# Kernel optimization log

Hardware: AMD Instinct MI355X
Metric: run time of the kernel (lower is better)

## Reference

```python
import jax, jax.numpy as jnp
import numpy as np
from jax import lax

N_NODES = 5000; N_EDGES = 160000; N_FEAT = 128; HIDDEN = 256
N_TPL = 10; N_TPL_NODES = 10; N_CLASSES = 8
ALPHA = 0.5          # FGW structure/feature trade-off
CG_ITERS = 5         # conditional-gradient (Frank-Wolfe) outer iterations
SINK_ITERS = 30      # log-domain Sinkhorn iterations (EMD surrogate)
SINK_REG = 0.02      # entropic reg relative to cost scale


def setup_inputs() -> dict:
    key = jax.random.key(0)
    ks = jax.random.split(key, 8)
    x = jax.random.normal(ks[0], (N_NODES, N_FEAT), jnp.float32)
    edge_index = jax.random.randint(ks[1], (2, N_EDGES), 0, N_NODES)
    W1 = jax.random.normal(ks[2], (N_FEAT, HIDDEN), jnp.float32) / np.sqrt(N_FEAT)
    b1 = jnp.zeros((HIDDEN,), jnp.float32)
    W2 = jax.random.normal(ks[3], (HIDDEN, N_FEAT), jnp.float32) / np.sqrt(HIDDEN)
    b2 = jnp.zeros((N_FEAT,), jnp.float32)
    templates = jax.random.uniform(ks[4], (N_TPL, N_TPL_NODES, N_TPL_NODES), jnp.float32)
    templates_features = jax.random.uniform(ks[5], (N_TPL, N_TPL_NODES, N_FEAT), jnp.float32)
    Wlin = jax.random.normal(ks[6], (N_TPL, N_CLASSES), jnp.float32) / np.sqrt(N_TPL)
    blin = jnp.zeros((N_CLASSES,), jnp.float32)
    return dict(x=x, edge_index=edge_index, W1=W1, b1=b1, W2=W2, b2=b2,
                templates=templates, templates_features=templates_features,
                Wlin=Wlin, blin=blin)


def gcn_conv(x, src, dst, W, b):
    # PyG GCNConv: x @ W, then D^-1/2 (A + I) D^-1/2 aggregation, then + b
    n = x.shape[0]
    loop = jnp.arange(n)
    s = jnp.concatenate([src, loop]); d = jnp.concatenate([dst, loop])
    deg = jax.ops.segment_sum(jnp.ones(s.shape[0], x.dtype), d, num_segments=n)
    dinv = lax.rsqrt(jnp.maximum(deg, 1.0))
    h = x @ W
    msg = h[s] * (dinv[s] * dinv[d])[:, None]
    return jax.ops.segment_sum(msg, d, num_segments=n) + b


def sinkhorn_log(G, logp, logq):
    # entropic OT in log domain as a jit-friendly surrogate for exact EMD
    scale = lax.stop_gradient(jnp.max(jnp.abs(G)) + 1e-9)
    mlogK = -G / (SINK_REG * scale)          # [n, m]
    f0 = jnp.zeros(G.shape[0], G.dtype); g0 = jnp.zeros(G.shape[1], G.dtype)
    def body(carry, _):
        f, g = carry
        g = logq - jax.nn.logsumexp(mlogK + f[:, None], axis=0)
        f = logp - jax.nn.logsumexp(mlogK + g[None, :], axis=1)
        return (f, g), None
    (f, g), _ = lax.scan(body, (f0, g0), None, length=SINK_ITERS)
    return jnp.exp(f[:, None] + mlogK + g[None, :])


def fgw2(C1, x, C2, F2):
    # Fused Gromov-Wasserstein distance (square loss), uniform weights,
    # conditional-gradient with fixed step 2/(t+2) and Sinkhorn LP surrogate.
    n, m = C1.shape[0], C2.shape[0]
    p = jnp.full((n,), 1.0 / n, x.dtype); q = jnp.full((m,), 1.0 / m, x.dtype)
    logp = jnp.log(p); logq = jnp.log(q)
    # squared-euclidean feature cost  [n, m]
    M = jnp.sum(x * x, 1)[:, None] + jnp.sum(F2 * F2, 1)[None, :] - 2.0 * x @ F2.T
    # square-loss GW decomposition: f1=a^2, f2=b^2, h1=a, h2=2b
    constC = ((C1 * C1) @ p)[:, None] + ((C2 * C2) @ q)[None, :]
    def tens(T):
        return constC - C1 @ T @ (2.0 * C2).T
    T = p[:, None] * q[None, :]
    for t in range(CG_ITERS):
        grad = (1.0 - ALPHA) * M + 2.0 * ALPHA * tens(T)
        Tnew = sinkhorn_log(grad, logp, logq)
        T = T + (2.0 / (t + 2.0)) * (Tnew - T)
    return (1.0 - ALPHA) * jnp.sum(M * T) + ALPHA * jnp.sum(tens(T) * T)


def reference(x, edge_index, W1, b1, W2, b2, templates, templates_features, Wlin, blin):
    src, dst = edge_index[0], edge_index[1]
    h = jax.nn.relu(gcn_conv(x, src, dst, W1, b1))
    h = gcn_conv(h, src, dst, W2, b2)           # [N, F]
    n = x.shape[0]
    C = jnp.zeros((n, n), x.dtype).at[src, dst].set(1.0)   # dense adjacency
    dists = jax.vmap(lambda Ct, Ft: fgw2(C, h, Ct, Ft))(templates, templates_features)  # [K]
    return dists @ Wlin + blin                  # [num_classes]
```

## Files before the change

kernel.cpp:

```cpp
#include <hip/hip_runtime.h>
#include <cstdint>

#define NND 5000
#define NE 160000
#define NF 128
#define NH 256
#define NT 10
#define MT 10
#define NC 8
#define NMAT (NND*MT)
#define CG_ITERS 5
#define SINK_IT 30

#if __has_builtin(__builtin_amdgcn_update_dpp)
#define DPP_ADD(x, ctrl, rmask) \
    ((x) + __int_as_float(__builtin_amdgcn_update_dpp(0, __float_as_int(x), (ctrl), (rmask), 0xf, true)))
__device__ __forceinline__ float wave_sum63(float x) {
    x = DPP_ADD(x, 0x111, 0xf);
    x = DPP_ADD(x, 0x112, 0xf);
    x = DPP_ADD(x, 0x114, 0xf);
    x = DPP_ADD(x, 0x118, 0xf);
    x = DPP_ADD(x, 0x142, 0xa);
    x = DPP_ADD(x, 0x143, 0xc);
    return x;
}
#else
__device__ __forceinline__ float wave_sum63(float x) {
#pragma unroll
    for (int off = 32; off; off >>= 1) x += __shfl_xor(x, off);
    return x;
}
#endif

__device__ __forceinline__ float frcp(float x) {
#if __has_builtin(__builtin_amdgcn_rcpf)
    return __builtin_amdgcn_rcpf(x);
#else
    return 1.f / x;
#endif
}


__global__ void k_edge1(const int* __restrict__ src, const int* __restrict__ dst,
                        int* __restrict__ cntD, unsigned* __restrict__ bitmap,
                        int* __restrict__ cntS, unsigned char* __restrict__ keep) {
    for (int e = blockIdx.x*blockDim.x + threadIdx.x; e < NE; e += gridDim.x*blockDim.x) {
        int s = src[e], d = dst[e];
        atomicAdd(&cntD[d], 1);
        int key = s * NND + d;
        unsigned bit = 1u << (key & 31);
        unsigned old = atomicOr(&bitmap[key >> 5], bit);
        if (!(old & bit)) { keep[e] = 1; atomicAdd(&cntS[s], 1); }
        else keep[e] = 0;
    }
}

__global__ void k_exscan2(const int* __restrict__ cntD, int* __restrict__ rpD,
                          float* __restrict__ dinv,
                          const int* __restrict__ cntS, int* __restrict__ rpS,
                          float* __restrict__ c1row,
                          const float* __restrict__ tpl, float* __restrict__ c2row) {
    const int T = 1024;
    int tid = threadIdx.x;
    if (blockIdx.x == 2) {
        if (tid < NT * MT) {
            int t = tid / MT, j = tid % MT;
            float s = 0.f;
            for (int k = 0; k < MT; k++) { float v = tpl[t * 100 + j * 10 + k]; s += v * v; }
            c2row[tid] = s * (1.f / MT);
        }
        return;
    }
    const int* cnt = blockIdx.x ? cntS : cntD;
    int* rp = blockIdx.x ? rpS : rpD;
    int C = (NND + T - 1) / T;
    int begin = tid * C, end = begin + C; if (end > NND) end = NND; if (begin > NND) begin = NND;
    int s = 0;
    for (int i = begin; i < end; i++) s += cnt[i];
    __shared__ int part[1024];
    part[tid] = s; __syncthreads();
    for (int off = 1; off < T; off <<= 1) {
        int v = (tid >= off) ? part[tid - off] : 0;
        __syncthreads();
        part[tid] += v;
        __syncthreads();
    }
    int run = part[tid] - s;
    for (int i = begin; i < end; i++) { rp[i] = run; run += cnt[i]; }
    if (tid == T - 1) rp[NND] = part[T - 1];
    if (blockIdx.x == 0)
        for (int i = begin; i < end; i++) dinv[i] = rsqrtf((float)(cnt[i] + 1));
    else
        for (int i = begin; i < end; i++) c1row[i] = (float)cnt[i] * (1.f / NND);
}

__global__ void k_scatter2(const int* __restrict__ src, const int* __restrict__ dst,
                           const unsigned char* __restrict__ keep,
                           const int* __restrict__ rpD, int* __restrict__ cur1,
                           int* __restrict__ csrS, float* __restrict__ csrC,
                           const float* __restrict__ dinv,
                           const int* __restrict__ rpS, int* __restrict__ cur2,
                           int* __restrict__ csrD) {
    for (int e = blockIdx.x*blockDim.x + threadIdx.x; e < NE; e += gridDim.x*blockDim.x) {
        int s = src[e], d = dst[e];
        int pos = rpD[d] + atomicAdd(&cur1[d], 1);
        csrS[pos] = s;
        csrC[pos] = dinv[s] * dinv[d];
        if (keep[e]) {
            int p2 = rpS[s] + atomicAdd(&cur2[s], 1);
            csrD[p2] = d;
        }
    }
}


__global__ __launch_bounds__(256) void k_gemm(const float* __restrict__ A,
                                              const float* __restrict__ B,
                                              float* __restrict__ C, int M, int N, int K,
                                              const float* __restrict__ bias, int relu) {
    const int BM = 64, BN = 64, BK = 16;
    __shared__ float As[BK][BM + 1];
    __shared__ float Bs[BK][BN];
    int tid = threadIdx.x;
    int row0 = blockIdx.y * BM, col0 = blockIdx.x * BN;
    int tx = tid % 16, ty = tid / 16;
    float acc[4][4] = {};
    for (int k0 = 0; k0 < K; k0 += BK) {
#pragma unroll
        for (int l = 0; l < 4; l++) {
            int idx = tid + l * 256;
            int r = idx / BK, kk = idx % BK;
            int gr = row0 + r;
            As[kk][r] = (gr < M) ? A[(size_t)gr * K + k0 + kk] : 0.f;
        }
#pragma unroll
        for (int l = 0; l < 4; l++) {
            int idx = tid + l * 256;
            int kk = idx / BN, c = idx % BN;
            Bs[kk][c] = B[(size_t)(k0 + kk) * N + col0 + c];
        }
        __syncthreads();
#pragma unroll
        for (int kk = 0; kk < BK; kk++) {
            float a[4], b[4];
#pragma unroll
            for (int i = 0; i < 4; i++) a[i] = As[kk][ty * 4 + i];
#pragma unroll
            for (int j = 0; j < 4; j++) b[j] = Bs[kk][tx * 4 + j];
#pragma unroll
            for (int i = 0; i < 4; i++)
#pragma unroll
                for (int j = 0; j < 4; j++) acc[i][j] += a[i] * b[j];
        }
        __syncthreads();
    }
#pragma unroll
    for (int i = 0; i < 4; i++) {
        int gr = row0 + ty * 4 + i;
        if (gr < M) {
#pragma unroll
            for (int j = 0; j < 4; j++) {
                int gc = col0 + tx * 4 + j;
                float o = acc[i][j];
                if (bias) o += bias[gc];
                if (relu) o = fmaxf(o, 0.f);
                C[(size_t)gr * N + gc] = o;
            }
        }
    }
}

__global__ __launch_bounds__(128) void k_aggregate(const float* __restrict__ hin,
                            const float* __restrict__ bias,
                            float* __restrict__ hout, const int* __restrict__ rp,
                            const int* __restrict__ csrS, const float* __restrict__ csrC,
                            const float* __restrict__ dinv) {
    int v = blockIdx.x;
    int f = threadIdx.x;
    float dv = dinv[v];
    float acc = hin[(size_t)v * NF + f] * dv * dv;
    int e0 = rp[v], e1 = rp[v + 1];
    for (int e = e0; e < e1; e++)
        acc += hin[(size_t)csrS[e] * NF + f] * csrC[e];
    if (bias) acc += bias[f];
    hout[(size_t)v * NF + f] = acc;
}


__global__ __launch_bounds__(128) void k_M(const float* __restrict__ h,
                    const float* __restrict__ tplF,
                    float* __restrict__ Mout) {
    int i = blockIdx.x;
    int tid = threadIdx.x;
    int lane = tid & 63, w = tid >> 6;
    __shared__ float hrow[NF];
    __shared__ float part[2];
    float hv = h[(size_t)i * NF + tid];
    hrow[tid] = hv;
    float ps = wave_sum63(hv * hv);
    if (lane == 63) part[w] = ps;
    __syncthreads();
    float sx = part[0] + part[1];
    int c = tid;
    if (c < NT * MT) {
        const float* Fc = tplF + (size_t)c * NF;
        float dot = 0.f, nrm = 0.f;
        for (int f = 0; f < NF; f++) {
            float fv = Fc[f];
            dot = fmaf(hrow[f], fv, dot);
            nrm = fmaf(fv, fv, nrm);
        }
        int t = c / MT, j = c % MT;
        Mout[(size_t)t * NMAT + (size_t)i * MT + j] = sx + nrm - 2.f * dot;
    }
}

__global__ void k_Tinit(float* __restrict__ T) {
    for (int idx = blockIdx.x*blockDim.x + threadIdx.x; idx < NT * NMAT; idx += gridDim.x*blockDim.x)
        T[idx] = 1.f / (float)NMAT;
}


__global__ __launch_bounds__(256) void k_grad(const float* __restrict__ T, const float* __restrict__ Mm,
                                              const float* __restrict__ c1row, const float* __restrict__ c2row,
                                              const float* __restrict__ tpl,
                                              const int* __restrict__ rpS, const int* __restrict__ csrD,
                                              float* __restrict__ G, unsigned* __restrict__ scaleBits) {
    int t = blockIdx.y;
    int tid = threadIdx.x;
    __shared__ float tC2[100];
    if (tid < 100) tC2[tid] = 2.f * tpl[t * 100 + tid];
    __syncthreads();
    int i = blockIdx.x * 256 + tid;
    float amax = 0.f;
    if (i < NND) {
        const float* Tt = T + (size_t)t * NMAT;
        const float* Mt = Mm + (size_t)t * NMAT;
        float* Gt = G + (size_t)t * NMAT;
        float L[MT];
#pragma unroll
        for (int j = 0; j < MT; j++) L[j] = 0.f;
        int e0 = rpS[i], e1 = rpS[i + 1];
        for (int e = e0; e < e1; e++) {
            int k = csrD[e];
            const float* Tk = Tt + (size_t)k * MT;
#pragma unroll
            for (int j = 0; j < MT; j++) L[j] += Tk[j];
        }
        float c1 = c1row[i];
#pragma unroll
        for (int j = 0; j < MT; j++) {
            float s = 0.f;
#pragma unroll
            for (int k = 0; k < MT; k++) s += L[k] * tC2[j * 10 + k];
            float g = 0.5f * Mt[(size_t)i * MT + j] + (c1 + c2row[t * 10 + j] - s);
            Gt[(size_t)i * MT + j] = g;
            amax = fmaxf(amax, fabsf(g));
        }
    }
    __shared__ float red[256];
    red[tid] = amax; __syncthreads();
    for (int off = 128; off > 0; off >>= 1) {
        if (tid < off) red[tid] = fmaxf(red[tid], red[tid + off]);
        __syncthreads();
    }
    if (tid == 0) atomicMax(&scaleBits[t], __float_as_uint(red[0]));
}

__global__ __launch_bounds__(512)
__attribute__((amdgpu_waves_per_eu(1, 2)))
void k_sinkhorn(const float* __restrict__ G,
                const unsigned* __restrict__ scaleBits,
                float* __restrict__ T, float step) {
    int t = blockIdx.x;
    int tid = threadIdx.x;
    int lane = tid & 63, w = tid >> 6;
    float sc = __uint_as_float(scaleBits[t]) + 1e-9f;
    float inv = -1.f / (0.02f * sc);
    const float* Gt = G + (size_t)t * NMAT;
    float* Tt = T + (size_t)t * NMAT;

    __shared__ float wred[8][10];
    __shared__ float vbc[12];

    float Kf[10][10];
    float u[10];
#pragma unroll
    for (int r = 0; r < 10; r++) {
        int i = tid + r * 512;
        if (i < NND) {
            u[r] = 1.f;
            const float2* Gr = (const float2*)(Gt + (size_t)i * 10);
#pragma unroll
            for (int h = 0; h < 5; h++) {
                float2 g = Gr[h];
                Kf[r][2*h]   = __expf(g.x * inv);
                Kf[r][2*h+1] = __expf(g.y * inv);
            }
        } else {
            u[r] = 0.f;
#pragma unroll
            for (int j = 0; j < 10; j++) Kf[r][j] = 0.f;
        }
    }

    float vv[10];

    for (int it = 0; it < SINK_IT; it++) {
        float S[10];
#pragma unroll
        for (int j = 0; j < 10; j++) S[j] = 0.f;
#pragma unroll
        for (int r = 0; r < 10; r++) {
            float ur = u[r];
#pragma unroll
            for (int j = 0; j < 10; j++) S[j] = fmaf(Kf[r][j], ur, S[j]);
        }
#pragma unroll
        for (int j = 0; j < 10; j++) {
            float s = wave_sum63(S[j]);
            if (lane == 63) wred[w][j] = s;
        }
        __syncthreads();
        if (tid < 10) {
            float s = 0.f;
#pragma unroll
            for (int q = 0; q < 8; q++) s += wred[q][tid];
            vbc[tid] = 0.1f * frcp(fmaxf(s, 1e-30f));
        }
        __syncthreads();
#pragma unroll
        for (int j = 0; j < 10; j++) vv[j] = vbc[j];
#pragma unroll
        for (int r = 0; r < 10; r++) {
            float R = 0.f;
#pragma unroll
            for (int j = 0; j < 10; j++) R = fmaf(Kf[r][j], vv[j], R);
            u[r] = (tid + r * 512 < NND) ? (2e-4f * frcp(fmaxf(R, 1e-30f))) : 0.f;
        }
    }

#pragma unroll
    for (int r = 0; r < 10; r++) {
        int i = tid + r * 512;
        if (i < NND) {
            float ur = u[r];
            float2* Tr = (float2*)(Tt + (size_t)i * 10);
#pragma unroll
            for (int h = 0; h < 5; h++) {
                float2 v = Tr[h];
                v.x += step * (ur * Kf[r][2*h]   * vv[2*h]   - v.x);
                v.y += step * (ur * Kf[r][2*h+1] * vv[2*h+1] - v.y);
                Tr[h] = v;
            }
        }
    }
}


__global__ __launch_bounds__(256) void k_final(const float* __restrict__ T, const float* __restrict__ Mm,
                                               const float* __restrict__ c1row, const float* __restrict__ c2row,
                                               const float* __restrict__ tpl,
                                               const int* __restrict__ rpS, const int* __restrict__ csrD,
                                               double* __restrict__ dd) {
    int t = blockIdx.y;
    int tid = threadIdx.x;
    __shared__ float tC2[100];
    if (tid < 100) tC2[tid] = 2.f * tpl[t * 100 + tid];
    __syncthreads();
    int i = blockIdx.x * 256 + tid;
    double msum = 0.0, tsum = 0.0;
    if (i < NND) {
        const float* Tt = T + (size_t)t * NMAT;
        const float* Mt = Mm + (size_t)t * NMAT;
        float L[MT];
#pragma unroll
        for (int j = 0; j < MT; j++) L[j] = 0.f;
        int e0 = rpS[i], e1 = rpS[i + 1];
        for (int e = e0; e < e1; e++) {
            int k = csrD[e];
            const float* Tk = Tt + (size_t)k * MT;
#pragma unroll
            for (int j = 0; j < MT; j++) L[j] += Tk[j];
        }
        float c1 = c1row[i];
#pragma unroll
        for (int j = 0; j < MT; j++) {
            float s = 0.f;
#pragma unroll
            for (int k = 0; k < MT; k++) s += L[k] * tC2[j * 10 + k];
            float ts = c1 + c2row[t * 10 + j] - s;
            float Tv = Tt[(size_t)i * MT + j];
            msum += (double)(Mt[(size_t)i * MT + j] * Tv);
            tsum += (double)(ts * Tv);
        }
    }
    __shared__ double r1[256], r2[256];
    r1[tid] = msum; r2[tid] = tsum; __syncthreads();
    for (int off = 128; off > 0; off >>= 1) {
        if (tid < off) { r1[tid] += r1[tid + off]; r2[tid] += r2[tid + off]; }
        __syncthreads();
    }
    if (tid == 0) { atomicAdd(&dd[t * 2], r1[0]); atomicAdd(&dd[t * 2 + 1], r2[0]); }
}

__global__ void k_out(const double* __restrict__ dd, const float* __restrict__ Wlin,
                      const float* __restrict__ blin, float* __restrict__ out) {
    int tid = threadIdx.x;
    __shared__ float ds[NT];
    if (tid < NT) ds[tid] = 0.5f * (float)(dd[2 * tid] + dd[2 * tid + 1]);
    __syncthreads();
    if (tid < NC) {
        float o = blin[tid];
#pragma unroll
        for (int t = 0; t < NT; t++) o += ds[t] * Wlin[t * NC + tid];
        out[tid] = o;
    }
}


extern "C" void kernel_launch(void* const* d_in, const int* in_sizes, int n_in,
                              void* d_out, int out_size, void* d_ws, size_t ws_size,
                              hipStream_t stream) {
    const float* x    = (const float*)d_in[0];
    const int*   ei   = (const int*)d_in[1];
    const int*   src  = ei;
    const int*   dst  = ei + NE;
    const float* W1   = (const float*)d_in[2];
    const float* b1   = (const float*)d_in[3];
    const float* W2   = (const float*)d_in[4];
    const float* b2   = (const float*)d_in[5];
    const float* tpl  = (const float*)d_in[6];
    const float* tplF = (const float*)d_in[7];
    const float* Wlin = (const float*)d_in[8];
    const float* blin = (const float*)d_in[9];
    float* out = (float*)d_out;

    char* w = (char*)d_ws;
    size_t off = 0;
    auto alloc = [&](size_t b) -> char* {
        off = (off + 255) & ~(size_t)255;
        char* p = w + off; off += b; return p;
    };
    float* bufA = (float*)alloc((size_t)NND * NH * 4);
    float* bufB = (float*)alloc((size_t)NND * NH * 4);
    float* bufH = (float*)alloc((size_t)NND * NF * 4);
    float* Mm   = (float*)alloc((size_t)NT * NMAT * 4);
    float* T    = (float*)alloc((size_t)NT * NMAT * 4);
    float* G    = (float*)alloc((size_t)NT * NMAT * 4);
    int* cntD = (int*)alloc((size_t)NND * 4);
    int* cntS = (int*)alloc((size_t)NND * 4);
    int* cur1 = (int*)alloc((size_t)NND * 4);
    int* cur2 = (int*)alloc((size_t)NND * 4);
    double* dd = (double*)alloc((size_t)NT * 2 * 8);
    unsigned* scaleArr = (unsigned*)alloc((size_t)CG_ITERS * NT * 4);
    char* zend = w + off;
    unsigned* bitmap = (unsigned*)alloc((size_t)781250 * 4);
    int* rpD  = (int*)alloc((size_t)(NND + 1) * 4);
    int* rpS  = (int*)alloc((size_t)(NND + 1) * 4);
    int* csrS = (int*)alloc((size_t)NE * 4);
    float* csrC = (float*)alloc((size_t)NE * 4);
    int* csrD2 = (int*)alloc((size_t)NE * 4);
    unsigned char* keep = (unsigned char*)alloc((size_t)NE);
    float* dinv  = (float*)alloc((size_t)NND * 4);
    float* c1row = (float*)alloc((size_t)NND * 4);
    float* c2row = (float*)alloc((size_t)100 * 4);

    hipMemsetAsync(cntD, 0, (size_t)(zend - (char*)cntD), stream);
    hipMemsetAsync(bitmap, 0, (size_t)781250 * 4, stream);

    k_edge1<<<625, 256, 0, stream>>>(src, dst, cntD, bitmap, cntS, keep);
    k_exscan2<<<3, 1024, 0, stream>>>(cntD, rpD, dinv, cntS, rpS, c1row, tpl, c2row);
    k_scatter2<<<625, 256, 0, stream>>>(src, dst, keep, rpD, cur1, csrS, csrC, dinv,
                                        rpS, cur2, csrD2);

    k_aggregate<<<NND, NF, 0, stream>>>(x, nullptr, bufA, rpD, csrS, csrC, dinv);
    k_gemm<<<dim3(NH / 64, (NND + 63) / 64), 256, 0, stream>>>(bufA, W1, bufB, NND, NH, NF, b1, 1);
    k_gemm<<<dim3(NF / 64, (NND + 63) / 64), 256, 0, stream>>>(bufB, W2, bufA, NND, NF, NH, nullptr, 0);
    k_aggregate<<<NND, NF, 0, stream>>>(bufA, b2, bufH, rpD, csrS, csrC, dinv);

    k_M<<<NND, 128, 0, stream>>>(bufH, tplF, Mm);
    k_Tinit<<<1954, 256, 0, stream>>>(T);

    for (int t = 0; t < CG_ITERS; t++) {
        unsigned* sb = scaleArr + t * NT;
        k_grad<<<dim3(20, NT), 256, 0, stream>>>(T, Mm, c1row, c2row, tpl, rpS, csrD2, G, sb);
        float step = 2.f / (float)(t + 2);
        k_sinkhorn<<<NT, 512, 0, stream>>>(G, sb, T, step);
    }

    k_final<<<dim3(20, NT), 256, 0, stream>>>(T, Mm, c1row, c2row, tpl, rpS, csrD2, dd);
    k_out<<<1, 64, 0, stream>>>(dd, Wlin, blin, out);
}
```

Before: 688.6 us.

## Vectorize aggregation and M kernels, widen Sinkhorn blocks to 1024 threads

The aggregation kernel now handles 8 nodes per block, with 32 lanes per node each loading a float4, in place of one node per 128-thread block. The M kernel reads template features as float4. The Sinkhorn kernel grows to 1024 threads, each holding 5 rows in explicitly named registers instead of 10 rows in arrays, which halves the serial per-thread work on the critical path of 10 single-block launches. The risks are higher register pressure at 1024 threads and a longer 16-wave reduction. Padded rows now get a nonzero u, but their K is zero so this is harmless.

```diff
diff --git a/kernel.cpp b/kernel.cpp
--- a/kernel.cpp
+++ b/kernel.cpp
@@ -170,20 +170,32 @@
     }
 }
 
-__global__ __launch_bounds__(128) void k_aggregate(const float* __restrict__ hin,
+__global__ __launch_bounds__(256) void k_aggregate(const float4* __restrict__ hin4,
                             const float* __restrict__ bias,
-                            float* __restrict__ hout, const int* __restrict__ rp,
+                            float4* __restrict__ hout4, const int* __restrict__ rp,
                             const int* __restrict__ csrS, const float* __restrict__ csrC,
                             const float* __restrict__ dinv) {
-    int v = blockIdx.x;
-    int f = threadIdx.x;
+    int v = blockIdx.x * 8 + (threadIdx.x >> 5);
+    int l = threadIdx.x & 31;
     float dv = dinv[v];
-    float acc = hin[(size_t)v * NF + f] * dv * dv;
+    float sc = dv * dv;
+    float4 a = hin4[(size_t)v * 32 + l];
+    float4 acc = make_float4(a.x * sc, a.y * sc, a.z * sc, a.w * sc);
     int e0 = rp[v], e1 = rp[v + 1];
-    for (int e = e0; e < e1; e++)
-        acc += hin[(size_t)csrS[e] * NF + f] * csrC[e];
-    if (bias) acc += bias[f];
-    hout[(size_t)v * NF + f] = acc;
+    for (int e = e0; e < e1; e++) {
+        int s = csrS[e];
+        float c = csrC[e];
+        float4 hv = hin4[(size_t)s * 32 + l];
+        acc.x = fmaf(hv.x, c, acc.x);
+        acc.y = fmaf(hv.y, c, acc.y);
+        acc.z = fmaf(hv.z, c, acc.z);
+        acc.w = fmaf(hv.w, c, acc.w);
+    }
+    if (bias) {
+        float4 bb = ((const float4*)bias)[l];
+        acc.x += bb.x; acc.y += bb.y; acc.z += bb.z; acc.w += bb.w;
+    }
+    hout4[(size_t)v * 32 + l] = acc;
 }
 
 
@@ -203,12 +215,17 @@
     float sx = part[0] + part[1];
     int c = tid;
     if (c < NT * MT) {
-        const float* Fc = tplF + (size_t)c * NF;
+        const float4* Fc = (const float4*)(tplF + (size_t)c * NF);
+        const float4* hr = (const float4*)hrow;
         float dot = 0.f, nrm = 0.f;
-        for (int f = 0; f < NF; f++) {
-            float fv = Fc[f];
-            dot = fmaf(hrow[f], fv, dot);
-            nrm = fmaf(fv, fv, nrm);
+#pragma unroll 8
+        for (int f = 0; f < NF / 4; f++) {
+            float4 fv = Fc[f];
+            float4 hq = hr[f];
+            dot = fmaf(hq.x, fv.x, dot); dot = fmaf(hq.y, fv.y, dot);
+            dot = fmaf(hq.z, fv.z, dot); dot = fmaf(hq.w, fv.w, dot);
+            nrm = fmaf(fv.x, fv.x, nrm); nrm = fmaf(fv.y, fv.y, nrm);
+            nrm = fmaf(fv.z, fv.z, nrm); nrm = fmaf(fv.w, fv.w, nrm);
         }
         int t = c / MT, j = c % MT;
         Mout[(size_t)t * NMAT + (size_t)i * MT + j] = sx + nrm - 2.f * dot;
@@ -267,8 +284,54 @@
     if (tid == 0) atomicMax(&scaleBits[t], __float_as_uint(red[0]));
 }
 
-__global__ __launch_bounds__(512)
-__attribute__((amdgpu_waves_per_eu(1, 2)))
+
+#define SK_ROWS(X) X(0) X(1) X(2) X(3) X(4)
+
+#define SK_DECL(r) float K##r##f0,K##r##f1,K##r##f2,K##r##f3,K##r##f4, \
+                         K##r##f5,K##r##f6,K##r##f7,K##r##f8,K##r##f9, u##r;
+
+#define SK_INIT(r) { int i = tid + (r)*1024; \
+    if (i < NND) { \
+        const float2* Gr = (const float2*)(Gt + (size_t)i*10); \
+        float2 a=Gr[0], b=Gr[1], c=Gr[2], d=Gr[3], e=Gr[4]; \
+        K##r##f0=__expf(a.x*inv); K##r##f1=__expf(a.y*inv); \
+        K##r##f2=__expf(b.x*inv); K##r##f3=__expf(b.y*inv); \
+        K##r##f4=__expf(c.x*inv); K##r##f5=__expf(c.y*inv); \
+        K##r##f6=__expf(d.x*inv); K##r##f7=__expf(d.y*inv); \
+        K##r##f8=__expf(e.x*inv); K##r##f9=__expf(e.y*inv); \
+        u##r = 1.f; \
+    } else { \
+        K##r##f0=K##r##f1=K##r##f2=K##r##f3=K##r##f4=0.f; \
+        K##r##f5=K##r##f6=K##r##f7=K##r##f8=K##r##f9=0.f; \
+        u##r = 0.f; } }
+
+#define SK_COL(r) { float ur = u##r; \
+    S0=fmaf(K##r##f0,ur,S0); S1=fmaf(K##r##f1,ur,S1); \
+    S2=fmaf(K##r##f2,ur,S2); S3=fmaf(K##r##f3,ur,S3); \
+    S4=fmaf(K##r##f4,ur,S4); S5=fmaf(K##r##f5,ur,S5); \
+    S6=fmaf(K##r##f6,ur,S6); S7=fmaf(K##r##f7,ur,S7); \
+    S8=fmaf(K##r##f8,ur,S8); S9=fmaf(K##r##f9,ur,S9); }
+
+#define SK_RED(j) { float s = wave_sum63(S##j); if (lane == 63) wred[w][j] = s; }
+
+#define SK_ROW(r) { float R = 0.f; \
+    R=fmaf(K##r##f0,V0,R); R=fmaf(K##r##f1,V1,R); \
+    R=fmaf(K##r##f2,V2,R); R=fmaf(K##r##f3,V3,R); \
+    R=fmaf(K##r##f4,V4,R); R=fmaf(K##r##f5,V5,R); \
+    R=fmaf(K##r##f6,V6,R); R=fmaf(K##r##f7,V7,R); \
+    R=fmaf(K##r##f8,V8,R); R=fmaf(K##r##f9,V9,R); \
+    u##r = 2e-4f * frcp(fmaxf(R, 1e-30f)); }
+
+#define SK_TUPD(r) { int i = tid + (r)*1024; \
+    if (i < NND) { float ur = u##r; \
+        float2* Tr = (float2*)(Tt + (size_t)i*10); float2 v; \
+        v=Tr[0]; v.x+=step*(ur*K##r##f0*V0-v.x); v.y+=step*(ur*K##r##f1*V1-v.y); Tr[0]=v; \
+        v=Tr[1]; v.x+=step*(ur*K##r##f2*V2-v.x); v.y+=step*(ur*K##r##f3*V3-v.y); Tr[1]=v; \
+        v=Tr[2]; v.x+=step*(ur*K##r##f4*V4-v.x); v.y+=step*(ur*K##r##f5*V5-v.y); Tr[2]=v; \
+        v=Tr[3]; v.x+=step*(ur*K##r##f6*V6-v.x); v.y+=step*(ur*K##r##f7*V7-v.y); Tr[3]=v; \
+        v=Tr[4]; v.x+=step*(ur*K##r##f8*V8-v.x); v.y+=step*(ur*K##r##f9*V9-v.y); Tr[4]=v; } }
+
+__global__ __launch_bounds__(1024)
 void k_sinkhorn(const float* __restrict__ G,
                 const unsigned* __restrict__ scaleBits,
                 float* __restrict__ T, float step) {
@@ -280,81 +343,35 @@
     const float* Gt = G + (size_t)t * NMAT;
     float* Tt = T + (size_t)t * NMAT;
 
-    __shared__ float wred[8][10];
+    __shared__ float wred[16][10];
     __shared__ float vbc[12];
 
-    float Kf[10][10];
-    float u[10];
-#pragma unroll
-    for (int r = 0; r < 10; r++) {
-        int i = tid + r * 512;
-        if (i < NND) {
-            u[r] = 1.f;
-            const float2* Gr = (const float2*)(Gt + (size_t)i * 10);
-#pragma unroll
-            for (int h = 0; h < 5; h++) {
-                float2 g = Gr[h];
-                Kf[r][2*h]   = __expf(g.x * inv);
-                Kf[r][2*h+1] = __expf(g.y * inv);
-            }
-        } else {
-            u[r] = 0.f;
-#pragma unroll
-            for (int j = 0; j < 10; j++) Kf[r][j] = 0.f;
-        }
-    }
-
-    float vv[10];
+    SK_ROWS(SK_DECL)
+    SK_ROWS(SK_INIT)
+
+    float V0,V1,V2,V3,V4,V5,V6,V7,V8,V9;
+    V0=V1=V2=V3=V4=V5=V6=V7=V8=V9=0.f;
 
     for (int it = 0; it < SINK_IT; it++) {
-        float S[10];
-#pragma unroll
-        for (int j = 0; j < 10; j++) S[j] = 0.f;
-#pragma unroll
-        for (int r = 0; r < 10; r++) {
-            float ur = u[r];
-#pragma unroll
-            for (int j = 0; j < 10; j++) S[j] = fmaf(Kf[r][j], ur, S[j]);
-        }
-#pragma unroll
-        for (int j = 0; j < 10; j++) {
-            float s = wave_sum63(S[j]);
-            if (lane == 63) wred[w][j] = s;
-        }
+        float S0,S1,S2,S3,S4,S5,S6,S7,S8,S9;
+        S0=S1=S2=S3=S4=S5=S6=S7=S8=S9=0.f;
+        SK_ROWS(SK_COL)
+        SK_RED(0) SK_RED(1) SK_RED(2) SK_RED(3) SK_RED(4)
+        SK_RED(5) SK_RED(6) SK_RED(7) SK_RED(8) SK_RED(9)
         __syncthreads();
         if (tid < 10) {
             float s = 0.f;
 #pragma unroll
-            for (int q = 0; q < 8; q++) s += wred[q][tid];
+            for (int q = 0; q < 16; q++) s += wred[q][tid];
             vbc[tid] = 0.1f * frcp(fmaxf(s, 1e-30f));
         }
         __syncthreads();
-#pragma unroll
-        for (int j = 0; j < 10; j++) vv[j] = vbc[j];
-#pragma unroll
-        for (int r = 0; r < 10; r++) {
-            float R = 0.f;
-#pragma unroll
-            for (int j = 0; j < 10; j++) R = fmaf(Kf[r][j], vv[j], R);
-            u[r] = (tid + r * 512 < NND) ? (2e-4f * frcp(fmaxf(R, 1e-30f))) : 0.f;
-        }
-    }
-
-#pragma unroll
-    for (int r = 0; r < 10; r++) {
-        int i = tid + r * 512;
-        if (i < NND) {
-            float ur = u[r];
-            float2* Tr = (float2*)(Tt + (size_t)i * 10);
-#pragma unroll
-            for (int h = 0; h < 5; h++) {
-                float2 v = Tr[h];
-                v.x += step * (ur * Kf[r][2*h]   * vv[2*h]   - v.x);
-                v.y += step * (ur * Kf[r][2*h+1] * vv[2*h+1] - v.y);
-                Tr[h] = v;
-            }
-        }
-    }
+        V0=vbc[0]; V1=vbc[1]; V2=vbc[2]; V3=vbc[3]; V4=vbc[4];
+        V5=vbc[5]; V6=vbc[6]; V7=vbc[7]; V8=vbc[8]; V9=vbc[9];
+        SK_ROWS(SK_ROW)
+    }
+
+    SK_ROWS(SK_TUPD)
 }
 
 
@@ -474,10 +491,12 @@
     k_scatter2<<<625, 256, 0, stream>>>(src, dst, keep, rpD, cur1, csrS, csrC, dinv,
                                         rpS, cur2, csrD2);
 
-    k_aggregate<<<NND, NF, 0, stream>>>(x, nullptr, bufA, rpD, csrS, csrC, dinv);
+    k_aggregate<<<625, 256, 0, stream>>>((const float4*)x, nullptr, (float4*)bufA,
+                                         rpD, csrS, csrC, dinv);
     k_gemm<<<dim3(NH / 64, (NND + 63) / 64), 256, 0, stream>>>(bufA, W1, bufB, NND, NH, NF, b1, 1);
     k_gemm<<<dim3(NF / 64, (NND + 63) / 64), 256, 0, stream>>>(bufB, W2, bufA, NND, NF, NH, nullptr, 0);
-    k_aggregate<<<NND, NF, 0, stream>>>(bufA, b2, bufH, rpD, csrS, csrC, dinv);
+    k_aggregate<<<625, 256, 0, stream>>>((const float4*)bufA, b2, (float4*)bufH,
+                                         rpD, csrS, csrC, dinv);
 
     k_M<<<NND, 128, 0, stream>>>(bufH, tplF, Mm);
     k_Tinit<<<1954, 256, 0, stream>>>(T);
@@ -486,7 +505,7 @@
         unsigned* sb = scaleArr + t * NT;
         k_grad<<<dim3(20, NT), 256, 0, stream>>>(T, Mm, c1row, c2row, tpl, rpS, csrD2, G, sb);
         float step = 2.f / (float)(t + 2);
-        k_sinkhorn<<<NT, 512, 0, stream>>>(G, sb, T, step);
+        k_sinkhorn<<<NT, 1024, 0, stream>>>(G, sb, T, step);
     }
 
     k_final<<<dim3(20, NT), 256, 0, stream>>>(T, Mm, c1row, c2row, tpl, rpS, csrD2, dd);
```

New measurement: 705.7 us. 2.5% more time.

## Vectorize aggregation, fuse T init into k_M, fold output into k_final

Applied to the files above, without the earlier changes.

The aggregation kernel now handles 8 nodes per 256-thread block, with 32 lanes per node each loading float4. k_M uses float4 loads and also writes the uniform T initialisation, which removes the k_Tinit launch. k_final uses a last-block-done counter to compute the classifier output, which removes the k_out launch. The sinkhorn kernel's occupancy attribute changes to waves_per_eu(2,2) and its broadcast vector is read as float4. Fewer launches and wider memory accesses are the intent; the waves_per_eu change may force register spills in the register-heavy Sinkhorn kernel.

```diff
diff --git a/kernel.cpp b/kernel.cpp
--- a/kernel.cpp
+++ b/kernel.cpp
@@ -170,26 +170,38 @@
     }
 }
 
-__global__ __launch_bounds__(128) void k_aggregate(const float* __restrict__ hin,
+__global__ __launch_bounds__(256) void k_aggregate(const float4* __restrict__ hin4,
                             const float* __restrict__ bias,
-                            float* __restrict__ hout, const int* __restrict__ rp,
+                            float4* __restrict__ hout4, const int* __restrict__ rp,
                             const int* __restrict__ csrS, const float* __restrict__ csrC,
                             const float* __restrict__ dinv) {
-    int v = blockIdx.x;
-    int f = threadIdx.x;
+    int v = blockIdx.x * 8 + (threadIdx.x >> 5);
+    int l = threadIdx.x & 31;
     float dv = dinv[v];
-    float acc = hin[(size_t)v * NF + f] * dv * dv;
+    float sc = dv * dv;
+    float4 a = hin4[(size_t)v * 32 + l];
+    float4 acc = make_float4(a.x * sc, a.y * sc, a.z * sc, a.w * sc);
     int e0 = rp[v], e1 = rp[v + 1];
-    for (int e = e0; e < e1; e++)
-        acc += hin[(size_t)csrS[e] * NF + f] * csrC[e];
-    if (bias) acc += bias[f];
-    hout[(size_t)v * NF + f] = acc;
+    for (int e = e0; e < e1; e++) {
+        int s = csrS[e];
+        float c = csrC[e];
+        float4 hv = hin4[(size_t)s * 32 + l];
+        acc.x = fmaf(hv.x, c, acc.x);
+        acc.y = fmaf(hv.y, c, acc.y);
+        acc.z = fmaf(hv.z, c, acc.z);
+        acc.w = fmaf(hv.w, c, acc.w);
+    }
+    if (bias) {
+        float4 bb = ((const float4*)bias)[l];
+        acc.x += bb.x; acc.y += bb.y; acc.z += bb.z; acc.w += bb.w;
+    }
+    hout4[(size_t)v * 32 + l] = acc;
 }
 
 
 __global__ __launch_bounds__(128) void k_M(const float* __restrict__ h,
                     const float* __restrict__ tplF,
-                    float* __restrict__ Mout) {
+                    float* __restrict__ Mout, float* __restrict__ T) {
     int i = blockIdx.x;
     int tid = threadIdx.x;
     int lane = tid & 63, w = tid >> 6;
@@ -203,21 +215,22 @@
     float sx = part[0] + part[1];
     int c = tid;
     if (c < NT * MT) {
-        const float* Fc = tplF + (size_t)c * NF;
+        const float4* Fc = (const float4*)(tplF + (size_t)c * NF);
+        const float4* hr = (const float4*)hrow;
         float dot = 0.f, nrm = 0.f;
-        for (int f = 0; f < NF; f++) {
-            float fv = Fc[f];
-            dot = fmaf(hrow[f], fv, dot);
-            nrm = fmaf(fv, fv, nrm);
+#pragma unroll 8
+        for (int f = 0; f < NF / 4; f++) {
+            float4 fv = Fc[f];
+            float4 hq = hr[f];
+            dot = fmaf(hq.x, fv.x, dot); dot = fmaf(hq.y, fv.y, dot);
+            dot = fmaf(hq.z, fv.z, dot); dot = fmaf(hq.w, fv.w, dot);
+            nrm = fmaf(fv.x, fv.x, nrm); nrm = fmaf(fv.y, fv.y, nrm);
+            nrm = fmaf(fv.z, fv.z, nrm); nrm = fmaf(fv.w, fv.w, nrm);
         }
         int t = c / MT, j = c % MT;
         Mout[(size_t)t * NMAT + (size_t)i * MT + j] = sx + nrm - 2.f * dot;
-    }
-}
-
-__global__ void k_Tinit(float* __restrict__ T) {
-    for (int idx = blockIdx.x*blockDim.x + threadIdx.x; idx < NT * NMAT; idx += gridDim.x*blockDim.x)
-        T[idx] = 1.f / (float)NMAT;
+        T[(size_t)t * NMAT + (size_t)i * MT + j] = 1.f / (float)NMAT;
+    }
 }
 
 
@@ -267,8 +280,7 @@
     if (tid == 0) atomicMax(&scaleBits[t], __float_as_uint(red[0]));
 }
 
-__global__ __launch_bounds__(512)
-__attribute__((amdgpu_waves_per_eu(1, 2)))
+__global__ __attribute__((amdgpu_flat_work_group_size(512, 512), amdgpu_waves_per_eu(2, 2)))
 void k_sinkhorn(const float* __restrict__ G,
                 const unsigned* __restrict__ scaleBits,
                 float* __restrict__ T, float step) {
@@ -281,7 +293,7 @@
     float* Tt = T + (size_t)t * NMAT;
 
     __shared__ float wred[8][10];
-    __shared__ float vbc[12];
+    __shared__ float4 vbc4[3];
 
     float Kf[10][10];
     float u[10];
@@ -326,11 +338,15 @@
             float s = 0.f;
 #pragma unroll
             for (int q = 0; q < 8; q++) s += wred[q][tid];
-            vbc[tid] = 0.1f * frcp(fmaxf(s, 1e-30f));
-        }
-        __syncthreads();
-#pragma unroll
-        for (int j = 0; j < 10; j++) vv[j] = vbc[j];
+            ((float*)vbc4)[tid] = 0.1f * frcp(fmaxf(s, 1e-30f));
+        }
+        __syncthreads();
+        {
+            float4 a = vbc4[0], b = vbc4[1], c = vbc4[2];
+            vv[0]=a.x; vv[1]=a.y; vv[2]=a.z; vv[3]=a.w;
+            vv[4]=b.x; vv[5]=b.y; vv[6]=b.z; vv[7]=b.w;
+            vv[8]=c.x; vv[9]=c.y;
+        }
 #pragma unroll
         for (int r = 0; r < 10; r++) {
             float R = 0.f;
@@ -362,7 +378,10 @@
                                                const float* __restrict__ c1row, const float* __restrict__ c2row,
                                                const float* __restrict__ tpl,
                                                const int* __restrict__ rpS, const int* __restrict__ csrD,
-                                               double* __restrict__ dd) {
+                                               double* __restrict__ dd, int* __restrict__ done,
+                                               const float* __restrict__ Wlin,
+                                               const float* __restrict__ blin,
+                                               float* __restrict__ out) {
     int t = blockIdx.y;
     int tid = threadIdx.x;
     __shared__ float tC2[100];
@@ -401,20 +420,30 @@
         if (tid < off) { r1[tid] += r1[tid + off]; r2[tid] += r2[tid + off]; }
         __syncthreads();
     }
-    if (tid == 0) { atomicAdd(&dd[t * 2], r1[0]); atomicAdd(&dd[t * 2 + 1], r2[0]); }
-}
-
-__global__ void k_out(const double* __restrict__ dd, const float* __restrict__ Wlin,
-                      const float* __restrict__ blin, float* __restrict__ out) {
-    int tid = threadIdx.x;
-    __shared__ float ds[NT];
-    if (tid < NT) ds[tid] = 0.5f * (float)(dd[2 * tid] + dd[2 * tid + 1]);
-    __syncthreads();
-    if (tid < NC) {
-        float o = blin[tid];
-#pragma unroll
-        for (int t = 0; t < NT; t++) o += ds[t] * Wlin[t * NC + tid];
-        out[tid] = o;
+    if (tid == 0) {
+        atomicAdd(&dd[t * 2], r1[0]);
+        atomicAdd(&dd[t * 2 + 1], r2[0]);
+        __threadfence();
+        int prev = atomicAdd(done, 1);
+        if (prev == 20 * NT - 1) {
+            __threadfence();
+            float ds[NT];
+#pragma unroll
+            for (int k = 0; k < NT; k++) {
+                unsigned long long b0 = __hip_atomic_load((unsigned long long*)&dd[2*k],
+                                        __ATOMIC_RELAXED, __HIP_MEMORY_SCOPE_AGENT);
+                unsigned long long b1 = __hip_atomic_load((unsigned long long*)&dd[2*k+1],
+                                        __ATOMIC_RELAXED, __HIP_MEMORY_SCOPE_AGENT);
+                ds[k] = 0.5f * (float)(__longlong_as_double(b0) + __longlong_as_double(b1));
+            }
+#pragma unroll
+            for (int c = 0; c < NC; c++) {
+                float o = blin[c];
+#pragma unroll
+                for (int k = 0; k < NT; k++) o = fmaf(ds[k], Wlin[k * NC + c], o);
+                out[c] = o;
+            }
+        }
     }
 }
 
@@ -453,6 +482,7 @@
     int* cur1 = (int*)alloc((size_t)NND * 4);
     int* cur2 = (int*)alloc((size_t)NND * 4);
     double* dd = (double*)alloc((size_t)NT * 2 * 8);
+    int* done = (int*)alloc(4);
     unsigned* scaleArr = (unsigned*)alloc((size_t)CG_ITERS * NT * 4);
     char* zend = w + off;
     unsigned* bitmap = (unsigned*)alloc((size_t)781250 * 4);
@@ -474,13 +504,14 @@
     k_scatter2<<<625, 256, 0, stream>>>(src, dst, keep, rpD, cur1, csrS, csrC, dinv,
                                         rpS, cur2, csrD2);
 
-    k_aggregate<<<NND, NF, 0, stream>>>(x, nullptr, bufA, rpD, csrS, csrC, dinv);
+    k_aggregate<<<625, 256, 0, stream>>>((const float4*)x, nullptr, (float4*)bufA,
+                                         rpD, csrS, csrC, dinv);
     k_gemm<<<dim3(NH / 64, (NND + 63) / 64), 256, 0, stream>>>(bufA, W1, bufB, NND, NH, NF, b1, 1);
     k_gemm<<<dim3(NF / 64, (NND + 63) / 64), 256, 0, stream>>>(bufB, W2, bufA, NND, NF, NH, nullptr, 0);
-    k_aggregate<<<NND, NF, 0, stream>>>(bufA, b2, bufH, rpD, csrS, csrC, dinv);
-
-    k_M<<<NND, 128, 0, stream>>>(bufH, tplF, Mm);
-    k_Tinit<<<1954, 256, 0, stream>>>(T);
+    k_aggregate<<<625, 256, 0, stream>>>((const float4*)bufA, b2, (float4*)bufH,
+                                         rpD, csrS, csrC, dinv);
+
+    k_M<<<NND, 128, 0, stream>>>(bufH, tplF, Mm, T);
 
     for (int t = 0; t < CG_ITERS; t++) {
         unsigned* sb = scaleArr + t * NT;
@@ -489,6 +520,6 @@
         k_sinkhorn<<<NT, 512, 0, stream>>>(G, sb, T, step);
     }
 
-    k_final<<<dim3(20, NT), 256, 0, stream>>>(T, Mm, c1row, c2row, tpl, rpS, csrD2, dd);
-    k_out<<<1, 64, 0, stream>>>(dd, Wlin, blin, out);
-}
+    k_final<<<dim3(20, NT), 256, 0, stream>>>(T, Mm, c1row, c2row, tpl, rpS, csrD2,
+                                              dd, done, Wlin, blin, out);
+}
```

Result: no change. 687.7 us (-0.1%).
